# Kernel tuning notes

Measured on AMD Instinct MI355X. Metric: run time of the kernel, lower is better.

## Reference

```python
import jax, jax.numpy as jnp
import numpy as np

N = 100000   # nodes
E = 1600000  # edges
G = 64       # graphs in batch
IN = 5
H = 2        # GAT heads
HID = 64
NCLS = 4


def setup_inputs() -> dict:
    key = jax.random.key(0)
    ks = jax.random.split(key, 16)
    rn = lambda k, s: (jax.random.normal(k, s, dtype=jnp.float32) * 0.1)
    f32 = jnp.float32
    return {
        "x": jax.random.normal(ks[0], (N, IN), dtype=f32),
        "edge_index": jax.random.randint(ks[1], (2, E), 0, N),
        "batch": jnp.sort(jax.random.randint(ks[2], (N,), 0, G)),
        # GATConv(5 -> 64, heads=2, concat=True)
        "gat_w": rn(ks[3], (IN, H * HID)),
        "att_src": rn(ks[4], (H, HID)),
        "att_dst": rn(ks[5], (H, HID)),
        "gat_b": jnp.zeros((H * HID,), f32),
        "bn1_g": jnp.ones((H * HID,), f32), "bn1_b": jnp.zeros((H * HID,), f32),
        # SAGEConv(128 -> 64): lin_l (aggregated, with bias) + lin_r (root, no bias)
        "sage_wl": rn(ks[6], (H * HID, HID)), "sage_bl": jnp.zeros((HID,), f32),
        "sage_wr": rn(ks[7], (H * HID, HID)),
        "bn2_g": jnp.ones((HID,), f32), "bn2_b": jnp.zeros((HID,), f32),
        # GCNConv(64 -> 64)
        "gcn_w": rn(ks[8], (HID, HID)), "gcn_b": jnp.zeros((HID,), f32),
        "bn3_g": jnp.ones((HID,), f32), "bn3_b": jnp.zeros((HID,), f32),
        # classifier MLP 128 -> 64 -> 4
        "w1": rn(ks[9], (2 * HID, HID)), "b1": jnp.zeros((HID,), f32),
        "w2": rn(ks[10], (HID, NCLS)), "b2": jnp.zeros((NCLS,), f32),
    }


def _bn(h, g, b):
    # BatchNorm in training-stats mode (dropout is treated as eval/identity)
    m = h.mean(0)
    v = h.var(0)
    return (h - m) * jax.lax.rsqrt(v + 1e-5) * g + b


def _forward(x, edge_index, batch, gat_w, att_src, att_dst, gat_b, bn1_g, bn1_b,
             sage_wl, sage_bl, sage_wr, bn2_g, bn2_b, gcn_w, gcn_b, bn3_g, bn3_b,
             w1, b1, w2, b2):
    src, dst = edge_index[0], edge_index[1]  # message flows src -> dst

    # ---- GATConv (heads=2, concat) ----
    xw = (x @ gat_w).reshape(-1, H, HID)                  # [N,H,C]
    a_src = (xw * att_src).sum(-1)                        # [N,H]
    a_dst = (xw * att_dst).sum(-1)                        # [N,H]
    e = jax.nn.leaky_relu(a_src[src] + a_dst[dst], 0.2)   # [E,H]
    e_max = jax.ops.segment_max(e, dst, num_segments=N)
    e_max = jnp.where(jnp.isfinite(e_max), e_max, 0.0)
    ex = jnp.exp(e - e_max[dst])
    denom = jax.ops.segment_sum(ex, dst, num_segments=N)
    alpha = ex / (denom[dst] + 1e-16)                     # segment softmax over incoming edges
    h = jax.ops.segment_sum(xw[src] * alpha[:, :, None], dst, num_segments=N)
    h = h.reshape(-1, H * HID) + gat_b
    h = jax.nn.elu(_bn(h, bn1_g, bn1_b))

    # ---- SAGEConv (mean aggregation) ----
    deg = jax.ops.segment_sum(jnp.ones((E,), h.dtype), dst, num_segments=N)
    agg = jax.ops.segment_sum(h[src], dst, num_segments=N) / jnp.maximum(deg, 1.0)[:, None]
    h = agg @ sage_wl + sage_bl + h @ sage_wr
    h = jax.nn.elu(_bn(h, bn2_g, bn2_b))

    # ---- GCNConv (symmetric norm, self loops) ----
    hw = h @ gcn_w
    deg_sl = deg + 1.0  # degree with self loop
    dinv = jax.lax.rsqrt(deg_sl)
    msg = hw[src] * (dinv[src] * dinv[dst])[:, None]
    h = jax.ops.segment_sum(msg, dst, num_segments=N) + hw * (dinv * dinv)[:, None] + gcn_b
    h = jax.nn.elu(_bn(h, bn3_g, bn3_b))

    # ---- global mean + max pool over graphs ----
    cnt = jax.ops.segment_sum(jnp.ones((h.shape[0],), h.dtype), batch, num_segments=G)
    pmean = jax.ops.segment_sum(h, batch, num_segments=G) / jnp.maximum(cnt, 1.0)[:, None]
    pmax = jax.ops.segment_max(h, batch, num_segments=G)
    pmax = jnp.where(jnp.isfinite(pmax), pmax, 0.0)
    z = jnp.concatenate([pmean, pmax], axis=1)            # [G, 2*HID]

    # ---- classifier ----
    z = jax.nn.relu(z @ w1 + b1)
    return z @ w2 + b2                                    # [G, NCLS]


def reference(x, edge_index, batch, gat_w, att_src, att_dst, gat_b, bn1_g, bn1_b,
              sage_wl, sage_bl, sage_wr, bn2_g, bn2_b, gcn_w, gcn_b, bn3_g, bn3_b,
              w1, b1, w2, b2):
    return _forward(x, edge_index, batch, gat_w, att_src, att_dst, gat_b, bn1_g, bn1_b,
                    sage_wl, sage_bl, sage_wr, bn2_g, bn2_b, gcn_w, gcn_b, bn3_g, bn3_b,
                    w1, b1, w2, b2)
```

## Files before the change

### kernel.cpp

```cpp
#include <hip/hip_runtime.h>
#include <hip/hip_bf16.h>
#include <math.h>

#define NN 100000
#define NE 1600000
#define NG 64
#define F_IN 5
#define F1 128
#define F2 64
#define NCLS 4
#define NCHUNK 250
#define CH_E 6400
#define NBUCK ((NN + 255) / 256)
#define CAPB 6144

typedef unsigned short ushort;
typedef __bf16 bf16x8 __attribute__((ext_vector_type(8)));
typedef float f32x4 __attribute__((ext_vector_type(4)));

__device__ __forceinline__ ushort f2bf(float f) {
    unsigned u = __float_as_uint(f);
    u = (u + 0x7fffu + ((u >> 16) & 1u)) >> 16;
    return (ushort)u;
}
__device__ __forceinline__ float bf2f(ushort h) {
    return __uint_as_float(((unsigned)h) << 16);
}
__device__ __forceinline__ unsigned pack2bf(float a, float b) {
    return (unsigned)f2bf(a) | ((unsigned)f2bf(b) << 16);
}
__device__ __forceinline__ float lo_bf(unsigned p) { return __uint_as_float(p << 16); }
__device__ __forceinline__ float hi_bf(unsigned p) { return __uint_as_float(p & 0xffff0000u); }

__device__ __forceinline__ unsigned enc_f(float f) {
    unsigned b = __float_as_uint(f);
    return (b & 0x80000000u) ? ~b : (b | 0x80000000u);
}
__device__ __forceinline__ float dec_f(unsigned k) {
    unsigned b = (k & 0x80000000u) ? (k ^ 0x80000000u) : ~k;
    return __uint_as_float(b);
}
#define ENC_NEG_INF 0x007FFFFFu

__global__ void k_fill_u32(unsigned* p, unsigned v, int n) {
    int i = blockIdx.x * blockDim.x + threadIdx.x;
    if (i < n) p[i] = v;
}

__global__ void k_packfrag_dual(const float* __restrict__ wl, const float* __restrict__ wr,
                                ushort* __restrict__ frag) {
    int idx = blockIdx.x * 256 + threadIdx.x;
    if (idx >= 4 * 8 * 64 * 8) return;
    int e = idx & 7;
    int lane = (idx >> 3) & 63;
    int ct = (idx >> 9) & 7;
    int ks = idx >> 12;
    int k = ks * 32 + (lane >> 4) * 8 + e;
    int n = ct * 16 + (lane & 15);
    float val = (n < 64) ? wl[k * 64 + n] : wr[k * 64 + (n - 64)];
    frag[idx] = f2bf(val);
}

__global__ void k_packfrag_gcn(const float* __restrict__ wm, ushort* __restrict__ frag) {
    int idx = blockIdx.x * 256 + threadIdx.x;
    if (idx >= 2 * 4 * 64 * 8) return;
    int e = idx & 7;
    int lane = (idx >> 3) & 63;
    int ct = (idx >> 9) & 3;
    int ks = idx >> 11;
    int k = ks * 32 + (lane >> 4) * 8 + e;
    int n = ct * 16 + (lane & 15);
    frag[idx] = f2bf(wm[k * 64 + n]);
}

__global__ void k_hist(const int* __restrict__ ei, int* __restrict__ ghist) {
    __shared__ int lh[NBUCK];
    int c = blockIdx.x, t = threadIdx.x;
    for (int b = t; b < NBUCK; b += 256) lh[b] = 0;
    __syncthreads();
    int e0 = c * CH_E;
#pragma unroll
    for (int i = 0; i < CH_E / 256; i++) {
        int d = ei[NE + e0 + t + i * 256];
        atomicAdd(&lh[d >> 8], 1);
    }
    __syncthreads();
    for (int b = t; b < NBUCK; b += 256) ghist[c * NBUCK + b] = lh[b];
}

__global__ void k_bscan(int* __restrict__ ghist, int* __restrict__ btot) {
    __shared__ int sh[256];
    int b = blockIdx.x, t = threadIdx.x;
    int v = (t < NCHUNK) ? ghist[t * NBUCK + b] : 0;
    sh[t] = v;
    __syncthreads();
    for (int off = 1; off < 256; off <<= 1) {
        int u = (t >= off) ? sh[t - off] : 0;
        __syncthreads();
        sh[t] += u;
        __syncthreads();
    }
    if (t < NCHUNK) ghist[t * NBUCK + b] = sh[t] - v;
    if (t == 255) btot[b] = sh[255];
}

__global__ void k_bprefix(const int* __restrict__ btot, int* __restrict__ bbase,
                          int* __restrict__ rowptr) {
    __shared__ int sh[512];
    int t = threadIdx.x;
    int v = (t < NBUCK) ? btot[t] : 0;
    sh[t] = v;
    __syncthreads();
    for (int off = 1; off < 512; off <<= 1) {
        int u = (t >= off) ? sh[t - off] : 0;
        __syncthreads();
        sh[t] += u;
        __syncthreads();
    }
    if (t < NBUCK) bbase[t] = sh[t] - v;
    if (t == 0) { bbase[NBUCK] = NE; rowptr[NN] = NE; }
}

__global__ void k_scatter2(const int* __restrict__ ei, const int* __restrict__ ghist,
                           const int* __restrict__ bbase, unsigned* __restrict__ staged) {
    __shared__ int lcur[NBUCK];
    int c = blockIdx.x, t = threadIdx.x;
    for (int b = t; b < NBUCK; b += 256) lcur[b] = ghist[c * NBUCK + b] + bbase[b];
    __syncthreads();
    int e0 = c * CH_E;
#pragma unroll
    for (int i = 0; i < CH_E / 256; i++) {
        int e = e0 + t + i * 256;
        int s = ei[e];
        int d = ei[NE + e];
        int pos = atomicAdd(&lcur[d >> 8], 1);
        staged[pos] = (((unsigned)(d & 255)) << 17) | (unsigned)s;
    }
}

__global__ void k_bucket_sort(const unsigned* __restrict__ staged, const int* __restrict__ bbase,
                              int* __restrict__ rowptr, int* __restrict__ csr_src,
                              float* __restrict__ dinv) {
    __shared__ unsigned ein[CAPB];
    __shared__ unsigned sout[CAPB];
    __shared__ int lhist[256];
    __shared__ int lps[256];
    int b = blockIdx.x, t = threadIdx.x;
    int n0 = b * 256;
    int g0 = bbase[b];
    int m = bbase[b + 1] - g0;
    lhist[t] = 0;
    __syncthreads();
    if (m <= CAPB) {
        for (int i = t; i < m; i += 256) {
            unsigned u = staged[g0 + i];
            ein[i] = u;
            atomicAdd(&lhist[u >> 17], 1);
        }
        __syncthreads();
        if (n0 + t < NN) dinv[n0 + t] = rsqrtf((float)lhist[t] + 1.0f);
        lps[t] = lhist[t];
        __syncthreads();
        for (int off = 1; off < 256; off <<= 1) {
            int v = (t >= off) ? lps[t - off] : 0;
            __syncthreads();
            lps[t] += v;
            __syncthreads();
        }
        int excl = lps[t] - lhist[t];
        if (n0 + t < NN) rowptr[n0 + t] = g0 + excl;
        __syncthreads();
        lhist[t] = excl;
        __syncthreads();
        for (int i = t; i < m; i += 256) {
            unsigned u = ein[i];
            int pos = atomicAdd(&lhist[u >> 17], 1);
            sout[pos] = u & 0x1FFFFu;
        }
        __syncthreads();
        for (int i = t; i < m; i += 256) csr_src[g0 + i] = (int)sout[i];
    } else {
        for (int i = t; i < m; i += 256) {
            unsigned u = staged[g0 + i];
            atomicAdd(&lhist[u >> 17], 1);
        }
        __syncthreads();
        if (n0 + t < NN) dinv[n0 + t] = rsqrtf((float)lhist[t] + 1.0f);
        lps[t] = lhist[t];
        __syncthreads();
        for (int off = 1; off < 256; off <<= 1) {
            int v = (t >= off) ? lps[t - off] : 0;
            __syncthreads();
            lps[t] += v;
            __syncthreads();
        }
        int excl = lps[t] - lhist[t];
        if (n0 + t < NN) rowptr[n0 + t] = g0 + excl;
        __syncthreads();
        lhist[t] = excl;
        __syncthreads();
        for (int i = t; i < m; i += 256) {
            unsigned u = staged[g0 + i];
            int pos = atomicAdd(&lhist[u >> 17], 1);
            csr_src[g0 + pos] = (int)(u & 0x1FFFFu);
        }
    }
}

__global__ void k_xw(const float* __restrict__ x, const float* __restrict__ gw,
                     const float* __restrict__ aw_src, const float* __restrict__ aw_dst,
                     unsigned* __restrict__ xw32, float* __restrict__ a_src,
                     float* __restrict__ a_dst) {
    __shared__ float w[F_IN * F1];
    int t = threadIdx.x;
    for (int i = t; i < F_IN * F1; i += 256) w[i] = gw[i];
    int wv = t >> 6, lane = t & 63;
    int f0 = 2 * lane, f1 = 2 * lane + 1;
    float as0 = aw_src[f0], as1 = aw_src[f1];
    float ad0 = aw_dst[f0], ad1 = aw_dst[f1];
    __syncthreads();
    int nbase = blockIdx.x * 64;
    for (int it = 0; it < 16; it++) {
        int n = nbase + it * 4 + wv;
        if (n >= NN) break;
        float xs[F_IN];
#pragma unroll
        for (int j = 0; j < F_IN; j++) xs[j] = x[n * F_IN + j];
        float acc0 = 0.f, acc1 = 0.f;
#pragma unroll
        for (int j = 0; j < F_IN; j++) {
            acc0 += xs[j] * w[j * F1 + f0];
            acc1 += xs[j] * w[j * F1 + f1];
        }
        xw32[(size_t)n * 64 + lane] = pack2bf(acc0, acc1);
        float p = acc0 * as0 + acc1 * as1;
        float q = acc0 * ad0 + acc1 * ad1;
#pragma unroll
        for (int off = 1; off < 32; off <<= 1) {
            p += __shfl_xor(p, off);
            q += __shfl_xor(q, off);
        }
        if (lane == 0)  { a_src[n * 2 + 0] = p; a_dst[n * 2 + 0] = q; }
        if (lane == 32) { a_src[n * 2 + 1] = p; a_dst[n * 2 + 1] = q; }
    }
}

__global__ void k_gat_gather(const int* __restrict__ rowptr, const int* __restrict__ csr_src,
                             const float* __restrict__ a_src, const float* __restrict__ a_dst,
                             const unsigned* __restrict__ xw32, unsigned* __restrict__ h1p) {
    int n = blockIdx.x * 4 + (threadIdx.x >> 6);
    int lane = threadIdx.x & 63;
    if (n >= NN) return;
    int j0 = rowptr[n], j1 = rowptr[n + 1];
    int deg = j1 - j0;
    float ad0 = a_dst[n * 2 + 0], ad1 = a_dst[n * 2 + 1];
    float acc0 = 0.f, acc1 = 0.f;
    bool lo = (lane < 32);
    if (deg <= 64) {
        int sl = 0;
        float l0 = -INFINITY, l1 = -INFINITY;
        if (lane < deg) {
            sl = csr_src[j0 + lane];
            l0 = a_src[sl * 2 + 0] + ad0;
            l1 = a_src[sl * 2 + 1] + ad1;
            l0 = l0 > 0.f ? l0 : 0.2f * l0;
            l1 = l1 > 0.f ? l1 : 0.2f * l1;
        }
        float m0 = l0, m1 = l1;
#pragma unroll
        for (int off = 32; off > 0; off >>= 1) {
            m0 = fmaxf(m0, __shfl_xor(m0, off));
            m1 = fmaxf(m1, __shfl_xor(m1, off));
        }
        float e0 = 0.f, e1 = 0.f;
        if (lane < deg) { e0 = expf(l0 - m0); e1 = expf(l1 - m1); }
        float s0 = e0, s1 = e1;
#pragma unroll
        for (int off = 32; off > 0; off >>= 1) {
            s0 += __shfl_xor(s0, off);
            s1 += __shfl_xor(s1, off);
        }
        unsigned al = pack2bf(e0 / (s0 + 1e-16f), e1 / (s1 + 1e-16f));
        int e = 0;
        for (; e + 4 <= deg; e += 4) {
            int s0i = __shfl(sl, e + 0), s1i = __shfl(sl, e + 1),
                s2i = __shfl(sl, e + 2), s3i = __shfl(sl, e + 3);
            unsigned b0 = __shfl(al, e + 0), b1 = __shfl(al, e + 1),
                     b2 = __shfl(al, e + 2), b3 = __shfl(al, e + 3);
            unsigned p0 = xw32[(size_t)s0i * 64 + lane];
            unsigned p1 = xw32[(size_t)s1i * 64 + lane];
            unsigned p2 = xw32[(size_t)s2i * 64 + lane];
            unsigned p3 = xw32[(size_t)s3i * 64 + lane];
            float w0 = lo ? lo_bf(b0) : hi_bf(b0);
            float w1 = lo ? lo_bf(b1) : hi_bf(b1);
            float w2 = lo ? lo_bf(b2) : hi_bf(b2);
            float w3 = lo ? lo_bf(b3) : hi_bf(b3);
            acc0 = fmaf(lo_bf(p0), w0, acc0); acc1 = fmaf(hi_bf(p0), w0, acc1);
            acc0 = fmaf(lo_bf(p1), w1, acc0); acc1 = fmaf(hi_bf(p1), w1, acc1);
            acc0 = fmaf(lo_bf(p2), w2, acc0); acc1 = fmaf(hi_bf(p2), w2, acc1);
            acc0 = fmaf(lo_bf(p3), w3, acc0); acc1 = fmaf(hi_bf(p3), w3, acc1);
        }
        for (; e < deg; e++) {
            int s = __shfl(sl, e); unsigned b = __shfl(al, e);
            unsigned p = xw32[(size_t)s * 64 + lane];
            float w = lo ? lo_bf(b) : hi_bf(b);
            acc0 = fmaf(lo_bf(p), w, acc0);
            acc1 = fmaf(hi_bf(p), w, acc1);
        }
    } else {
        float m0 = -INFINITY, m1 = -INFINITY, s0 = 0.f, s1 = 0.f;
        for (int base = j0; base < j1; base += 64) {
            int myj = base + lane;
            float l0 = -INFINITY, l1 = -INFINITY;
            if (myj < j1) {
                int s = csr_src[myj];
                l0 = a_src[s * 2 + 0] + ad0;
                l1 = a_src[s * 2 + 1] + ad1;
                l0 = l0 > 0.f ? l0 : 0.2f * l0;
                l1 = l1 > 0.f ? l1 : 0.2f * l1;
            }
            float cm0 = l0, cm1 = l1;
#pragma unroll
            for (int off = 32; off > 0; off >>= 1) {
                cm0 = fmaxf(cm0, __shfl_xor(cm0, off));
                cm1 = fmaxf(cm1, __shfl_xor(cm1, off));
            }
            float nm0 = fmaxf(m0, cm0), nm1 = fmaxf(m1, cm1);
            float ce0 = (myj < j1) ? expf(l0 - nm0) : 0.f;
            float ce1 = (myj < j1) ? expf(l1 - nm1) : 0.f;
            float cs0 = ce0, cs1 = ce1;
#pragma unroll
            for (int off = 32; off > 0; off >>= 1) {
                cs0 += __shfl_xor(cs0, off);
                cs1 += __shfl_xor(cs1, off);
            }
            s0 = s0 * expf(m0 - nm0) + cs0;
            s1 = s1 * expf(m1 - nm1) + cs1;
            m0 = nm0; m1 = nm1;
        }
        float r0 = 1.0f / (s0 + 1e-16f), r1 = 1.0f / (s1 + 1e-16f);
        for (int base = j0; base < j1; base += 64) {
            int cnt = min(64, j1 - base);
            int myj = base + lane;
            int sl = 0; unsigned al = 0;
            if (myj < j1) {
                sl = csr_src[myj];
                float l0 = a_src[sl * 2 + 0] + ad0;
                float l1 = a_src[sl * 2 + 1] + ad1;
                l0 = l0 > 0.f ? l0 : 0.2f * l0;
                l1 = l1 > 0.f ? l1 : 0.2f * l1;
                al = pack2bf(expf(l0 - m0) * r0, expf(l1 - m1) * r1);
            }
            int e = 0;
            for (; e + 4 <= cnt; e += 4) {
                int s0i = __shfl(sl, e + 0), s1i = __shfl(sl, e + 1),
                    s2i = __shfl(sl, e + 2), s3i = __shfl(sl, e + 3);
                unsigned b0 = __shfl(al, e + 0), b1 = __shfl(al, e + 1),
                         b2 = __shfl(al, e + 2), b3 = __shfl(al, e + 3);
                unsigned p0 = xw32[(size_t)s0i * 64 + lane];
                unsigned p1 = xw32[(size_t)s1i * 64 + lane];
                unsigned p2 = xw32[(size_t)s2i * 64 + lane];
                unsigned p3 = xw32[(size_t)s3i * 64 + lane];
                float w0 = lo ? lo_bf(b0) : hi_bf(b0);
                float w1 = lo ? lo_bf(b1) : hi_bf(b1);
                float w2 = lo ? lo_bf(b2) : hi_bf(b2);
                float w3 = lo ? lo_bf(b3) : hi_bf(b3);
                acc0 = fmaf(lo_bf(p0), w0, acc0); acc1 = fmaf(hi_bf(p0), w0, acc1);
                acc0 = fmaf(lo_bf(p1), w1, acc0); acc1 = fmaf(hi_bf(p1), w1, acc1);
                acc0 = fmaf(lo_bf(p2), w2, acc0); acc1 = fmaf(hi_bf(p2), w2, acc1);
                acc0 = fmaf(lo_bf(p3), w3, acc0); acc1 = fmaf(hi_bf(p3), w3, acc1);
            }
            for (; e < cnt; e++) {
                int s = __shfl(sl, e); unsigned b = __shfl(al, e);
                unsigned p = xw32[(size_t)s * 64 + lane];
                float w = lo ? lo_bf(b) : hi_bf(b);
                acc0 = fmaf(lo_bf(p), w, acc0);
                acc1 = fmaf(hi_bf(p), w, acc1);
            }
        }
    }
    h1p[(size_t)n * 64 + lane] = pack2bf(acc0, acc1);
}

__global__ void k_bn_stats_bf(const ushort* __restrict__ h, int nfeat, float* __restrict__ sums) {
    __shared__ float sh[512];
    int t = threadIdx.x;
    int f = t & (nfeat - 1);
    int rg = t / nfeat;
    int R = 256 / nfeat;
    int rows = (NN + gridDim.x - 1) / gridDim.x;
    int rbase = blockIdx.x * rows;
    int r1 = min(NN, rbase + rows);
    float s = 0.f, ss = 0.f;
    for (int r = rbase + rg; r < r1; r += R) {
        float v = bf2f(h[(size_t)r * nfeat + f]);
        s += v; ss += v * v;
    }
    sh[t] = s; sh[256 + t] = ss;
    __syncthreads();
    if (rg == 0) {
        for (int g = 1; g < R; g++) {
            s += sh[g * nfeat + f];
            ss += sh[256 + g * nfeat + f];
        }
        atomicAdd(&sums[f], s);
        atomicAdd(&sums[nfeat + f], ss);
    }
}

__global__ void k_bn_apply_bf(const ushort* __restrict__ h, const float* __restrict__ sums,
                              const float* __restrict__ g, const float* __restrict__ b,
                              int nfeat, int total, ushort* __restrict__ hb) {
    int i = blockIdx.x * blockDim.x + threadIdx.x;
    if (i >= total) return;
    int f = i & (nfeat - 1);
    float m = sums[f] * (1.0f / NN);
    float var = sums[nfeat + f] * (1.0f / NN) - m * m;
    float v = (bf2f(h[i]) - m) * rsqrtf(var + 1e-5f) * g[f] + b[f];
    hb[i] = f2bf(v > 0.f ? v : expm1f(v));
}

__global__ void k_sage_dualgemm(const ushort* __restrict__ h1b, const ushort* __restrict__ fragd,
                                ushort* __restrict__ u_bf, float* __restrict__ v) {
    __shared__ uint4 sfrag[2048];
    int t = threadIdx.x;
    const uint4* f4 = (const uint4*)fragd;
    for (int i = t; i < 2048; i += 256) sfrag[i] = f4[i];
    __syncthreads();
    int w = t >> 6, lane = t & 63;
    int row0 = blockIdx.x * 64 + w * 16;
    int arow = row0 + (lane & 15);
    if (arow >= NN) arow = NN - 1;
    f32x4 acc[8];
#pragma unroll
    for (int c = 0; c < 8; c++) acc[c] = (f32x4){0.f, 0.f, 0.f, 0.f};
#pragma unroll
    for (int ks = 0; ks < 4; ks++) {
        union { uint4 u; bf16x8 f; } ua;
        ua.u = *(const uint4*)&h1b[(size_t)arow * F1 + ks * 32 + (lane >> 4) * 8];
#pragma unroll
        for (int ct = 0; ct < 8; ct++) {
            union { uint4 u; bf16x8 f; } ub;
            ub.u = sfrag[(ks * 8 + ct) * 64 + lane];
            acc[ct] = __builtin_amdgcn_mfma_f32_16x16x32_bf16(ua.f, ub.f, acc[ct], 0, 0, 0);
        }
    }
    int mrow0 = row0 + (lane >> 4) * 4;
    int n = lane & 15;
#pragma unroll
    for (int reg = 0; reg < 4; reg++) {
        int r = mrow0 + reg;
        if (r >= NN) continue;
#pragma unroll
        for (int ct = 0; ct < 4; ct++)
            u_bf[(size_t)r * F2 + ct * 16 + n] = f2bf(acc[ct][reg]);
#pragma unroll
        for (int ct = 4; ct < 8; ct++)
            v[(size_t)r * F2 + (ct - 4) * 16 + n] = acc[ct][reg];
    }
}

__global__ void k_sage_gather2(const int* __restrict__ rowptr, const int* __restrict__ csr_src,
                               const ushort* __restrict__ u_bf, const float* __restrict__ v,
                               const float* __restrict__ bl, ushort* __restrict__ h2bf) {
    int n = blockIdx.x * 4 + (threadIdx.x >> 6);
    int lane = threadIdx.x & 63;
    if (n >= NN) return;
    int j0 = rowptr[n], j1 = rowptr[n + 1];
    float a = 0.f;
    for (int base = j0; base < j1; base += 64) {
        int cnt = min(64, j1 - base);
        int myj = base + lane;
        int sl = (myj < j1) ? csr_src[myj] : 0;
        int e = 0;
        for (; e + 4 <= cnt; e += 4) {
            int s0 = __shfl(sl, e + 0), s1 = __shfl(sl, e + 1),
                s2 = __shfl(sl, e + 2), s3 = __shfl(sl, e + 3);
            float t0 = bf2f(u_bf[(size_t)s0 * F2 + lane]);
            float t1 = bf2f(u_bf[(size_t)s1 * F2 + lane]);
            float t2 = bf2f(u_bf[(size_t)s2 * F2 + lane]);
            float t3 = bf2f(u_bf[(size_t)s3 * F2 + lane]);
            a += (t0 + t1) + (t2 + t3);
        }
        for (; e < cnt; e++) {
            int s = __shfl(sl, e);
            a += bf2f(u_bf[(size_t)s * F2 + lane]);
        }
    }
    float inv = 1.0f / fmaxf((float)(j1 - j0), 1.0f);
    h2bf[(size_t)n * F2 + lane] = f2bf(a * inv + v[(size_t)n * F2 + lane] + bl[lane]);
}

__global__ void k_gcn_gemm(const ushort* __restrict__ h2b, const ushort* __restrict__ fragg,
                           const float* __restrict__ dinv, ushort* __restrict__ hwd_bf) {
    __shared__ uint4 sfrag[512];
    int t = threadIdx.x;
    const uint4* f4 = (const uint4*)fragg;
    for (int i = t; i < 512; i += 256) sfrag[i] = f4[i];
    __syncthreads();
    int w = t >> 6, lane = t & 63;
    int row0 = blockIdx.x * 64 + w * 16;
    int arow = row0 + (lane & 15);
    if (arow >= NN) arow = NN - 1;
    f32x4 acc[4];
#pragma unroll
    for (int c = 0; c < 4; c++) acc[c] = (f32x4){0.f, 0.f, 0.f, 0.f};
#pragma unroll
    for (int ks = 0; ks < 2; ks++) {
        union { uint4 u; bf16x8 f; } ua;
        ua.u = *(const uint4*)&h2b[(size_t)arow * F2 + ks * 32 + (lane >> 4) * 8];
#pragma unroll
        for (int ct = 0; ct < 4; ct++) {
            union { uint4 u; bf16x8 f; } ub;
            ub.u = sfrag[(ks * 4 + ct) * 64 + lane];
            acc[ct] = __builtin_amdgcn_mfma_f32_16x16x32_bf16(ua.f, ub.f, acc[ct], 0, 0, 0);
        }
    }
    int mrow0 = row0 + (lane >> 4) * 4;
    int n = lane & 15;
#pragma unroll
    for (int reg = 0; reg < 4; reg++) {
        int r = mrow0 + reg;
        if (r >= NN) continue;
        float d = dinv[r];
#pragma unroll
        for (int ct = 0; ct < 4; ct++)
            hwd_bf[(size_t)r * F2 + ct * 16 + n] = f2bf(acc[ct][reg] * d);
    }
}

__global__ void k_gcn_gather(const int* __restrict__ rowptr, const int* __restrict__ csr_src,
                             const ushort* __restrict__ hwd_bf, const float* __restrict__ dinv,
                             const float* __restrict__ gb, ushort* __restrict__ h3bf) {
    int n = blockIdx.x * 4 + (threadIdx.x >> 6);
    int lane = threadIdx.x & 63;
    if (n >= NN) return;
    int j0 = rowptr[n], j1 = rowptr[n + 1];
    float acc = 0.f;
    for (int base = j0; base < j1; base += 64) {
        int cnt = min(64, j1 - base);
        int myj = base + lane;
        int sl = (myj < j1) ? csr_src[myj] : 0;
        int e = 0;
        for (; e + 4 <= cnt; e += 4) {
            int s0 = __shfl(sl, e + 0), s1 = __shfl(sl, e + 1),
                s2 = __shfl(sl, e + 2), s3 = __shfl(sl, e + 3);
            float t0 = bf2f(hwd_bf[(size_t)s0 * F2 + lane]);
            float t1 = bf2f(hwd_bf[(size_t)s1 * F2 + lane]);
            float t2 = bf2f(hwd_bf[(size_t)s2 * F2 + lane]);
            float t3 = bf2f(hwd_bf[(size_t)s3 * F2 + lane]);
            acc += (t0 + t1) + (t2 + t3);
        }
        for (; e < cnt; e++) {
            int s = __shfl(sl, e);
            acc += bf2f(hwd_bf[(size_t)s * F2 + lane]);
        }
    }
    float di = dinv[n];
    acc += bf2f(hwd_bf[(size_t)n * F2 + lane]);
    h3bf[(size_t)n * F2 + lane] = f2bf(acc * di + gb[lane]);
}

__global__ void k_bn3_pool(const ushort* __restrict__ h3bf, const float* __restrict__ sums,
                           const float* __restrict__ g3, const float* __restrict__ b3,
                           const int* __restrict__ batch, float* __restrict__ psum,
                           unsigned* __restrict__ pmax, float* __restrict__ cnt) {
    int w = threadIdx.x >> 6;
    int lane = threadIdx.x & 63;
    int chunk = blockIdx.x * 4 + w;
    int nchunks = gridDim.x * 4;
    int rows = (NN + nchunks - 1) / nchunks;
    int r0 = chunk * rows;
    int r1 = min(NN, r0 + rows);
    if (r0 >= r1) return;
    float m = sums[lane] * (1.0f / NN);
    float var = sums[F2 + lane] * (1.0f / NN) - m * m;
    float sc = rsqrtf(var + 1e-5f) * g3[lane];
    float bb = b3[lane];
    int curg = batch[r0];
    float ls = 0.f, lm = -INFINITY;
    int run = 0;
    for (int r = r0; r < r1; r++) {
        int gg = batch[r];
        if (gg != curg) {
            atomicAdd(&psum[curg * F2 + lane], ls);
            atomicMax(&pmax[curg * F2 + lane], enc_f(lm));
            if (lane == 0) atomicAdd(&cnt[curg], (float)run);
            curg = gg; ls = 0.f; lm = -INFINITY; run = 0;
        }
        float v = (bf2f(h3bf[(size_t)r * F2 + lane]) - m) * sc + bb;
        v = v > 0.f ? v : expm1f(v);
        ls += v; lm = fmaxf(lm, v); run++;
    }
    atomicAdd(&psum[curg * F2 + lane], ls);
    atomicMax(&pmax[curg * F2 + lane], enc_f(lm));
    if (lane == 0) atomicAdd(&cnt[curg], (float)run);
}

__global__ void k_cls(const float* __restrict__ psum, const unsigned* __restrict__ pmax,
                      const float* __restrict__ cnt, const float* __restrict__ w1,
                      const float* __restrict__ b1, const float* __restrict__ w2,
                      const float* __restrict__ b2, float* __restrict__ out) {
    int g = blockIdx.x;
    int j = threadIdx.x;
    __shared__ float z[2 * F2];
    __shared__ float hid[F2];
    float c = fmaxf(cnt[g], 1.0f);
    z[j] = psum[g * F2 + j] / c;
    float mv = dec_f(pmax[g * F2 + j]);
    z[F2 + j] = isfinite(mv) ? mv : 0.f;
    __syncthreads();
    float acc = b1[j];
#pragma unroll 8
    for (int k = 0; k < 2 * F2; k++) acc += z[k] * w1[k * F2 + j];
    hid[j] = fmaxf(acc, 0.f);
    __syncthreads();
    if (j < NCLS) {
        float o = b2[j];
#pragma unroll 8
        for (int k = 0; k < F2; k++) o += hid[k] * w2[k * NCLS + j];
        out[g * NCLS + j] = o;
    }
}

extern "C" void kernel_launch(void* const* d_in, const int* in_sizes, int n_in,
                              void* d_out, int out_size, void* d_ws, size_t ws_size,
                              hipStream_t stream) {
    const float* x       = (const float*)d_in[0];
    const int*   ei      = (const int*)d_in[1];
    const int*   batch   = (const int*)d_in[2];
    const float* gat_w   = (const float*)d_in[3];
    const float* att_src = (const float*)d_in[4];
    const float* att_dst = (const float*)d_in[5];
    const float* bn1_g   = (const float*)d_in[7];
    const float* bn1_b   = (const float*)d_in[8];
    const float* sage_wl = (const float*)d_in[9];
    const float* sage_bl = (const float*)d_in[10];
    const float* sage_wr = (const float*)d_in[11];
    const float* bn2_g   = (const float*)d_in[12];
    const float* bn2_b   = (const float*)d_in[13];
    const float* gcn_w   = (const float*)d_in[14];
    const float* gcn_b   = (const float*)d_in[15];
    const float* bn3_g   = (const float*)d_in[16];
    const float* bn3_b   = (const float*)d_in[17];
    const float* w1      = (const float*)d_in[18];
    const float* b1      = (const float*)d_in[19];
    const float* w2      = (const float*)d_in[20];
    const float* b2      = (const float*)d_in[21];
    float* out = (float*)d_out;

    float* ws = (float*)d_ws;
    size_t o_A    = 0;
    size_t o_h1   = o_A   + (size_t)NN * F1;
    size_t o_h2   = o_h1  + (size_t)NN * F1;
    size_t o_csr  = o_h2  + (size_t)NN * F2;
    size_t o_rp   = o_csr + (size_t)NE;
    size_t o_bb   = o_rp  + (size_t)(NN + 4);
    size_t o_bt   = o_bb  + 400;
    size_t o_asrc = o_bt  + 400;
    size_t o_adst = o_asrc + (size_t)NN * 2;
    size_t o_dinv = o_adst + (size_t)NN * 2;
    size_t o_sums = o_dinv + (size_t)NN;
    size_t o_frd  = o_sums + 768;
    size_t o_frg  = o_frd  + 8192;
    size_t o_psum = o_frg  + 2048;
    size_t o_cnt  = o_psum + (size_t)NG * F2;
    size_t o_pmax = o_cnt  + (size_t)NG;

    float* A    = ws + o_A;
    float* h1r  = ws + o_h1;
    float* h2r  = ws + o_h2;
    int* csr_src = (int*)(ws + o_csr);
    int* rowptr  = (int*)(ws + o_rp);
    int* bbase   = (int*)(ws + o_bb);
    int* btot    = (int*)(ws + o_bt);
    float* asr  = ws + o_asrc;
    float* ads  = ws + o_adst;
    float* dinv = ws + o_dinv;
    float* sums1 = ws + o_sums;
    float* sums2 = sums1 + 256;
    float* sums3 = sums2 + 256;
    ushort* fragd = (ushort*)(ws + o_frd);
    ushort* fragg = (ushort*)(ws + o_frg);
    float* psum = ws + o_psum;
    float* cnt  = ws + o_cnt;
    unsigned* pmax = (unsigned*)(ws + o_pmax);

    unsigned* staged = (unsigned*)A;
    int*    ghist  = (int*)(A + 2 * 1024 * 1024);
    unsigned* xw32 = (unsigned*)A;
    ushort* u_bf   = (ushort*)A;
    float*  vmat   = A + (size_t)NN * F2 / 2;
    ushort* hwd_bf = (ushort*)A;
    ushort* h3bf   = (ushort*)(A + (size_t)NN * F2 / 2);
    unsigned* h1p  = (unsigned*)h1r;
    ushort* h1bf   = (ushort*)h1r;
    ushort* h1b    = (ushort*)h2r;
    ushort* h2bf   = (ushort*)h2r;
    ushort* h2b    = (ushort*)h1r;

    hipMemsetAsync(sums1, 0, sizeof(float) * 768, stream);
    hipMemsetAsync(psum, 0, sizeof(float) * (NG * F2 + NG), stream);
    k_fill_u32<<<(NG * F2 + 255) / 256, 256, 0, stream>>>(pmax, ENC_NEG_INF, NG * F2);

    k_hist<<<NCHUNK, 256, 0, stream>>>(ei, ghist);
    k_bscan<<<NBUCK, 256, 0, stream>>>(ghist, btot);
    k_bprefix<<<1, 512, 0, stream>>>(btot, bbase, rowptr);
    k_scatter2<<<NCHUNK, 256, 0, stream>>>(ei, ghist, bbase, staged);
    k_bucket_sort<<<NBUCK, 256, 0, stream>>>(staged, bbase, rowptr, csr_src, dinv);

    k_xw<<<(NN + 63) / 64, 256, 0, stream>>>(x, gat_w, att_src, att_dst, xw32, asr, ads);
    k_gat_gather<<<(NN + 3) / 4, 256, 0, stream>>>(rowptr, csr_src, asr, ads, xw32, h1p);
    k_bn_stats_bf<<<1024, 256, 0, stream>>>(h1bf, F1, sums1);
    k_bn_apply_bf<<<(NN * F1 + 255) / 256, 256, 0, stream>>>(h1bf, sums1, bn1_g, bn1_b,
                                                             F1, NN * F1, h1b);

    k_packfrag_dual<<<(16384 + 255) / 256, 256, 0, stream>>>(sage_wl, sage_wr, fragd);
    k_sage_dualgemm<<<(NN + 63) / 64, 256, 0, stream>>>(h1b, fragd, u_bf, vmat);
    k_sage_gather2<<<(NN + 3) / 4, 256, 0, stream>>>(rowptr, csr_src, u_bf, vmat, sage_bl, h2bf);
    k_bn_stats_bf<<<1024, 256, 0, stream>>>(h2bf, F2, sums2);
    k_bn_apply_bf<<<(NN * F2 + 255) / 256, 256, 0, stream>>>(h2bf, sums2, bn2_g, bn2_b,
                                                             F2, NN * F2, h2b);

    k_packfrag_gcn<<<(4096 + 255) / 256, 256, 0, stream>>>(gcn_w, fragg);
    k_gcn_gemm<<<(NN + 63) / 64, 256, 0, stream>>>(h2b, fragg, dinv, hwd_bf);
    k_gcn_gather<<<(NN + 3) / 4, 256, 0, stream>>>(rowptr, csr_src, hwd_bf, dinv, gcn_b, h3bf);
    k_bn_stats_bf<<<1024, 256, 0, stream>>>(h3bf, F2, sums3);

    k_bn3_pool<<<1024, 256, 0, stream>>>(h3bf, sums3, bn3_g, bn3_b, batch, psum, pmax, cnt);
    k_cls<<<NG, F2, 0, stream>>>(psum, pmax, cnt, w1, b1, w2, b2, out);
}
```

Measured before the change: 474.9 us.

## Fuse BatchNorm+ELU apply into SAGE and GCN GEMM loads; merge init and packfrag kernels

Removes the two standalone BN-apply kernels. Each GEMM now computes per-feature scale and shift from the stats sums into shared memory and applies BN plus ELU to its A-operand while loading. The memset, fill and two weight-pack launches are merged into single kernels, and the SAGE root-term matrix is stored as bf16 instead of fp32. This saves roughly two full read-write passes over the hidden activations and several launches, at the cost of extra ALU work in the GEMMs and slightly lower precision in the root term.

```diff
diff --git a/kernel.cpp b/kernel.cpp
--- a/kernel.cpp
+++ b/kernel.cpp
@@ -31,6 +31,7 @@
 }
 __device__ __forceinline__ float lo_bf(unsigned p) { return __uint_as_float(p << 16); }
 __device__ __forceinline__ float hi_bf(unsigned p) { return __uint_as_float(p & 0xffff0000u); }
+__device__ __forceinline__ float eluf(float z) { return z > 0.f ? z : expm1f(z); }
 
 __device__ __forceinline__ unsigned enc_f(float f) {
     unsigned b = __float_as_uint(f);
@@ -42,35 +43,37 @@
 }
 #define ENC_NEG_INF 0x007FFFFFu
 
-__global__ void k_fill_u32(unsigned* p, unsigned v, int n) {
-    int i = blockIdx.x * blockDim.x + threadIdx.x;
-    if (i < n) p[i] = v;
-}
-
-__global__ void k_packfrag_dual(const float* __restrict__ wl, const float* __restrict__ wr,
-                                ushort* __restrict__ frag) {
+__global__ void k_init(float* __restrict__ sums, float* __restrict__ psum_cnt,
+                       unsigned* __restrict__ pmax) {
+    int i = blockIdx.x * 256 + threadIdx.x;
+    if (i < 768) sums[i] = 0.f;
+    if (i < NG * F2 + NG) psum_cnt[i] = 0.f;
+    if (i < NG * F2) pmax[i] = ENC_NEG_INF;
+}
+
+__global__ void k_packfrag(const float* __restrict__ wl, const float* __restrict__ wr,
+                           const float* __restrict__ wg,
+                           ushort* __restrict__ fragd, ushort* __restrict__ fragg) {
     int idx = blockIdx.x * 256 + threadIdx.x;
-    if (idx >= 4 * 8 * 64 * 8) return;
-    int e = idx & 7;
-    int lane = (idx >> 3) & 63;
-    int ct = (idx >> 9) & 7;
-    int ks = idx >> 12;
-    int k = ks * 32 + (lane >> 4) * 8 + e;
-    int n = ct * 16 + (lane & 15);
-    float val = (n < 64) ? wl[k * 64 + n] : wr[k * 64 + (n - 64)];
-    frag[idx] = f2bf(val);
-}
-
-__global__ void k_packfrag_gcn(const float* __restrict__ wm, ushort* __restrict__ frag) {
-    int idx = blockIdx.x * 256 + threadIdx.x;
-    if (idx >= 2 * 4 * 64 * 8) return;
-    int e = idx & 7;
-    int lane = (idx >> 3) & 63;
-    int ct = (idx >> 9) & 3;
-    int ks = idx >> 11;
-    int k = ks * 32 + (lane >> 4) * 8 + e;
-    int n = ct * 16 + (lane & 15);
-    frag[idx] = f2bf(wm[k * 64 + n]);
+    if (idx < 16384) {
+        int e = idx & 7;
+        int lane = (idx >> 3) & 63;
+        int ct = (idx >> 9) & 7;
+        int ks = idx >> 12;
+        int k = ks * 32 + (lane >> 4) * 8 + e;
+        int n = ct * 16 + (lane & 15);
+        float val = (n < 64) ? wl[k * 64 + n] : wr[k * 64 + (n - 64)];
+        fragd[idx] = f2bf(val);
+    } else if (idx < 16384 + 4096) {
+        int j = idx - 16384;
+        int e = j & 7;
+        int lane = (j >> 3) & 63;
+        int ct = (j >> 9) & 3;
+        int ks = j >> 11;
+        int k = ks * 32 + (lane >> 4) * 8 + e;
+        int n = ct * 16 + (lane & 15);
+        fragg[j] = f2bf(wg[k * 64 + n]);
+    }
 }
 
 __global__ void k_hist(const int* __restrict__ ei, int* __restrict__ ghist) {
@@ -408,24 +411,22 @@
     }
 }
 
-__global__ void k_bn_apply_bf(const ushort* __restrict__ h, const float* __restrict__ sums,
-                              const float* __restrict__ g, const float* __restrict__ b,
-                              int nfeat, int total, ushort* __restrict__ hb) {
-    int i = blockIdx.x * blockDim.x + threadIdx.x;
-    if (i >= total) return;
-    int f = i & (nfeat - 1);
-    float m = sums[f] * (1.0f / NN);
-    float var = sums[nfeat + f] * (1.0f / NN) - m * m;
-    float v = (bf2f(h[i]) - m) * rsqrtf(var + 1e-5f) * g[f] + b[f];
-    hb[i] = f2bf(v > 0.f ? v : expm1f(v));
-}
-
-__global__ void k_sage_dualgemm(const ushort* __restrict__ h1b, const ushort* __restrict__ fragd,
-                                ushort* __restrict__ u_bf, float* __restrict__ v) {
+__global__ void k_sage_dualgemm(const ushort* __restrict__ h1bf, const float* __restrict__ sums,
+                                const float* __restrict__ g, const float* __restrict__ b,
+                                const ushort* __restrict__ fragd,
+                                ushort* __restrict__ u_bf, ushort* __restrict__ v_bf) {
     __shared__ uint4 sfrag[2048];
+    __shared__ float sco[F1], ssh[F1];
     int t = threadIdx.x;
     const uint4* f4 = (const uint4*)fragd;
     for (int i = t; i < 2048; i += 256) sfrag[i] = f4[i];
+    if (t < F1) {
+        float m = sums[t] * (1.0f / NN);
+        float var = sums[F1 + t] * (1.0f / NN) - m * m;
+        float sc = rsqrtf(var + 1e-5f) * g[t];
+        sco[t] = sc;
+        ssh[t] = b[t] - m * sc;
+    }
     __syncthreads();
     int w = t >> 6, lane = t & 63;
     int row0 = blockIdx.x * 64 + w * 16;
@@ -436,8 +437,21 @@
     for (int c = 0; c < 8; c++) acc[c] = (f32x4){0.f, 0.f, 0.f, 0.f};
 #pragma unroll
     for (int ks = 0; ks < 4; ks++) {
+        int kb = ks * 32 + (lane >> 4) * 8;
+        uint4 raw = *(const uint4*)&h1bf[(size_t)arow * F1 + kb];
         union { uint4 u; bf16x8 f; } ua;
-        ua.u = *(const uint4*)&h1b[(size_t)arow * F1 + ks * 32 + (lane >> 4) * 8];
+        {
+            float e0 = eluf(fmaf(lo_bf(raw.x), sco[kb + 0], ssh[kb + 0]));
+            float e1 = eluf(fmaf(hi_bf(raw.x), sco[kb + 1], ssh[kb + 1]));
+            float e2 = eluf(fmaf(lo_bf(raw.y), sco[kb + 2], ssh[kb + 2]));
+            float e3 = eluf(fmaf(hi_bf(raw.y), sco[kb + 3], ssh[kb + 3]));
+            float e4 = eluf(fmaf(lo_bf(raw.z), sco[kb + 4], ssh[kb + 4]));
+            float e5 = eluf(fmaf(hi_bf(raw.z), sco[kb + 5], ssh[kb + 5]));
+            float e6 = eluf(fmaf(lo_bf(raw.w), sco[kb + 6], ssh[kb + 6]));
+            float e7 = eluf(fmaf(hi_bf(raw.w), sco[kb + 7], ssh[kb + 7]));
+            ua.u.x = pack2bf(e0, e1); ua.u.y = pack2bf(e2, e3);
+            ua.u.z = pack2bf(e4, e5); ua.u.w = pack2bf(e6, e7);
+        }
 #pragma unroll
         for (int ct = 0; ct < 8; ct++) {
             union { uint4 u; bf16x8 f; } ub;
@@ -456,12 +470,12 @@
             u_bf[(size_t)r * F2 + ct * 16 + n] = f2bf(acc[ct][reg]);
 #pragma unroll
         for (int ct = 4; ct < 8; ct++)
-            v[(size_t)r * F2 + (ct - 4) * 16 + n] = acc[ct][reg];
+            v_bf[(size_t)r * F2 + (ct - 4) * 16 + n] = f2bf(acc[ct][reg]);
     }
 }
 
 __global__ void k_sage_gather2(const int* __restrict__ rowptr, const int* __restrict__ csr_src,
-                               const ushort* __restrict__ u_bf, const float* __restrict__ v,
+                               const ushort* __restrict__ u_bf, const ushort* __restrict__ v_bf,
                                const float* __restrict__ bl, ushort* __restrict__ h2bf) {
     int n = blockIdx.x * 4 + (threadIdx.x >> 6);
     int lane = threadIdx.x & 63;
@@ -488,15 +502,25 @@
         }
     }
     float inv = 1.0f / fmaxf((float)(j1 - j0), 1.0f);
-    h2bf[(size_t)n * F2 + lane] = f2bf(a * inv + v[(size_t)n * F2 + lane] + bl[lane]);
-}
-
-__global__ void k_gcn_gemm(const ushort* __restrict__ h2b, const ushort* __restrict__ fragg,
+    h2bf[(size_t)n * F2 + lane] = f2bf(a * inv + bf2f(v_bf[(size_t)n * F2 + lane]) + bl[lane]);
+}
+
+__global__ void k_gcn_gemm(const ushort* __restrict__ h2bf, const float* __restrict__ sums,
+                           const float* __restrict__ g, const float* __restrict__ b,
+                           const ushort* __restrict__ fragg,
                            const float* __restrict__ dinv, ushort* __restrict__ hwd_bf) {
     __shared__ uint4 sfrag[512];
+    __shared__ float sco[F2], ssh[F2];
     int t = threadIdx.x;
     const uint4* f4 = (const uint4*)fragg;
     for (int i = t; i < 512; i += 256) sfrag[i] = f4[i];
+    if (t < F2) {
+        float m = sums[t] * (1.0f / NN);
+        float var = sums[F2 + t] * (1.0f / NN) - m * m;
+        float sc = rsqrtf(var + 1e-5f) * g[t];
+        sco[t] = sc;
+        ssh[t] = b[t] - m * sc;
+    }
     __syncthreads();
     int w = t >> 6, lane = t & 63;
     int row0 = blockIdx.x * 64 + w * 16;
@@ -507,8 +531,21 @@
     for (int c = 0; c < 4; c++) acc[c] = (f32x4){0.f, 0.f, 0.f, 0.f};
 #pragma unroll
     for (int ks = 0; ks < 2; ks++) {
+        int kb = ks * 32 + (lane >> 4) * 8;
+        uint4 raw = *(const uint4*)&h2bf[(size_t)arow * F2 + kb];
         union { uint4 u; bf16x8 f; } ua;
-        ua.u = *(const uint4*)&h2b[(size_t)arow * F2 + ks * 32 + (lane >> 4) * 8];
+        {
+            float e0 = eluf(fmaf(lo_bf(raw.x), sco[kb + 0], ssh[kb + 0]));
+            float e1 = eluf(fmaf(hi_bf(raw.x), sco[kb + 1], ssh[kb + 1]));
+            float e2 = eluf(fmaf(lo_bf(raw.y), sco[kb + 2], ssh[kb + 2]));
+            float e3 = eluf(fmaf(hi_bf(raw.y), sco[kb + 3], ssh[kb + 3]));
+            float e4 = eluf(fmaf(lo_bf(raw.z), sco[kb + 4], ssh[kb + 4]));
+            float e5 = eluf(fmaf(hi_bf(raw.z), sco[kb + 5], ssh[kb + 5]));
+            float e6 = eluf(fmaf(lo_bf(raw.w), sco[kb + 6], ssh[kb + 6]));
+            float e7 = eluf(fmaf(hi_bf(raw.w), sco[kb + 7], ssh[kb + 7]));
+            ua.u.x = pack2bf(e0, e1); ua.u.y = pack2bf(e2, e3);
+            ua.u.z = pack2bf(e4, e5); ua.u.w = pack2bf(e6, e7);
+        }
 #pragma unroll
         for (int ct = 0; ct < 4; ct++) {
             union { uint4 u; bf16x8 f; } ub;
@@ -690,18 +727,14 @@
     int*    ghist  = (int*)(A + 2 * 1024 * 1024);
     unsigned* xw32 = (unsigned*)A;
     ushort* u_bf   = (ushort*)A;
-    float*  vmat   = A + (size_t)NN * F2 / 2;
+    ushort* v_bf   = (ushort*)(A + (size_t)NN * F2 / 2);
     ushort* hwd_bf = (ushort*)A;
     ushort* h3bf   = (ushort*)(A + (size_t)NN * F2 / 2);
     unsigned* h1p  = (unsigned*)h1r;
     ushort* h1bf   = (ushort*)h1r;
-    ushort* h1b    = (ushort*)h2r;
     ushort* h2bf   = (ushort*)h2r;
-    ushort* h2b    = (ushort*)h1r;
-
-    hipMemsetAsync(sums1, 0, sizeof(float) * 768, stream);
-    hipMemsetAsync(psum, 0, sizeof(float) * (NG * F2 + NG), stream);
-    k_fill_u32<<<(NG * F2 + 255) / 256, 256, 0, stream>>>(pmax, ENC_NEG_INF, NG * F2);
+
+    k_init<<<(NG * F2 + NG + 255) / 256 + 1, 256, 0, stream>>>(sums1, psum, pmax);
 
     k_hist<<<NCHUNK, 256, 0, stream>>>(ei, ghist);
     k_bscan<<<NBUCK, 256, 0, stream>>>(ghist, btot);
@@ -712,18 +745,17 @@
     k_xw<<<(NN + 63) / 64, 256, 0, stream>>>(x, gat_w, att_src, att_dst, xw32, asr, ads);
     k_gat_gather<<<(NN + 3) / 4, 256, 0, stream>>>(rowptr, csr_src, asr, ads, xw32, h1p);
     k_bn_stats_bf<<<1024, 256, 0, stream>>>(h1bf, F1, sums1);
-    k_bn_apply_bf<<<(NN * F1 + 255) / 256, 256, 0, stream>>>(h1bf, sums1, bn1_g, bn1_b,
-                                                             F1, NN * F1, h1b);
-
-    k_packfrag_dual<<<(16384 + 255) / 256, 256, 0, stream>>>(sage_wl, sage_wr, fragd);
-    k_sage_dualgemm<<<(NN + 63) / 64, 256, 0, stream>>>(h1b, fragd, u_bf, vmat);
-    k_sage_gather2<<<(NN + 3) / 4, 256, 0, stream>>>(rowptr, csr_src, u_bf, vmat, sage_bl, h2bf);
+
+    k_packfrag<<<(16384 + 4096 + 255) / 256, 256, 0, stream>>>(sage_wl, sage_wr, gcn_w,
+                                                               fragd, fragg);
+    k_sage_dualgemm<<<(NN + 63) / 64, 256, 0, stream>>>(h1bf, sums1, bn1_g, bn1_b,
+                                                        fragd, u_bf, v_bf);
+    k_sage_gather2<<<(NN + 3) / 4, 256, 0, stream>>>(rowptr, csr_src, u_bf, v_bf,
+                                                     sage_bl, h2bf);
     k_bn_stats_bf<<<1024, 256, 0, stream>>>(h2bf, F2, sums2);
-    k_bn_apply_bf<<<(NN * F2 + 255) / 256, 256, 0, stream>>>(h2bf, sums2, bn2_g, bn2_b,
-                                                             F2, NN * F2, h2b);
-
-    k_packfrag_gcn<<<(4096 + 255) / 256, 256, 0, stream>>>(gcn_w, fragg);
-    k_gcn_gemm<<<(NN + 63) / 64, 256, 0, stream>>>(h2b, fragg, dinv, hwd_bf);
+
+    k_gcn_gemm<<<(NN + 63) / 64, 256, 0, stream>>>(h2bf, sums2, bn2_g, bn2_b,
+                                                   fragg, dinv, hwd_bf);
     k_gcn_gather<<<(NN + 3) / 4, 256, 0, stream>>>(rowptr, csr_src, hwd_bf, dinv, gcn_b, h3bf);
     k_bn_stats_bf<<<1024, 256, 0, stream>>>(h3bf, F2, sums3);
 
```

New measurement: 445.2 us. 6.3% less time.
